# Performance work log

Measured on AMD Instinct MI355X. Metric: run time of the kernel, lower is better.

## Reference

```python
import jax, jax.numpy as jnp
import numpy as np

EPS = 1e-8  # torch F.cosine_similarity norm clamp


def setup_inputs() -> dict:
    key = jax.random.key(0)
    kq, km = jax.random.split(key)
    b, c, h, w = 4, 128, 16, 16
    n_mem = 2000
    query_feature = jax.random.normal(kq, (b, c, h, w), dtype=jnp.float32)
    memory_bank = jax.random.normal(km, (n_mem, b, c, h, w), dtype=jnp.float32)
    return {"query_feature": query_feature, "memory_bank": memory_bank, "k": 20}


def reference(query_feature, memory_bank, k):
    b = query_feature.shape[0]
    n = memory_bank.shape[0]
    # Flatten per-batch features: query [b, D], memory [N, b, D]
    qf = query_feature.reshape(b, -1)
    mf = memory_bank.reshape(n, b, -1)
    # Cosine similarity along feature dim (torch clamps each norm by eps)
    qn = qf / jnp.maximum(jnp.linalg.norm(qf, axis=-1, keepdims=True), EPS)
    mn = mf / jnp.maximum(jnp.linalg.norm(mf, axis=-1, keepdims=True), EPS)
    sims = jnp.einsum('bd,nbd->n', qn, mn) / b  # mean over batch -> [N]
    top_vals, top_idx = jax.lax.top_k(sims, k)
    weights = jax.nn.softmax(top_vals)  # [k]
    # Weighted gather-sum of selected memory items -> [b, c, h, w]
    selected = memory_bank[top_idx]  # [k, b, c, h, w]
    weighted_sum = jnp.einsum('k,kbchw->bchw', weights, selected)
    return weighted_sum
```

## Files before the change

### kernel.cpp

```cpp
#include <hip/hip_runtime.h>
#include <hip/hip_bf16.h>
#include <math.h>

#define BQ    4
#define DIM   32768
#define DIM4  8192
#define ITEM4 32768
#define EPS   1e-8f

__global__ void qnorm_kernel(const float* __restrict__ q, float* __restrict__ qn2) {
    const int b = blockIdx.x;
    const float4* q4 = (const float4*)(q + (size_t)b * DIM);
    float nrm = 0.f;
    for (int i = threadIdx.x; i < DIM4; i += blockDim.x) {
        float4 v = q4[i];
        nrm += v.x * v.x + v.y * v.y + v.z * v.z + v.w * v.w;
    }
    for (int off = 32; off > 0; off >>= 1) nrm += __shfl_down(nrm, off);
    __shared__ float s[16];
    const int wid = threadIdx.x >> 6;
    if ((threadIdx.x & 63) == 0) s[wid] = nrm;
    __syncthreads();
    if (threadIdx.x == 0) {
        float tot = 0.f;
        for (int w = 0; w < (int)(blockDim.x >> 6); ++w) tot += s[w];
        qn2[b] = tot;
    }
}

#define QREG 16
__global__ __launch_bounds__(512) void dot_norm_kernel(
        const float* __restrict__ q, const float* __restrict__ mem,
        float* __restrict__ dotv, float* __restrict__ mn2v, int N) {
    const int b    = blockIdx.x & 3;
    const int bn   = blockIdx.x >> 2;
    const int nblk = gridDim.x >> 2;

    const float4* q4 = (const float4*)(q + (size_t)b * DIM);
    float4 qr[QREG];
    #pragma unroll
    for (int j = 0; j < QREG; ++j) qr[j] = q4[threadIdx.x + j * 512];

    __shared__ float sd[8], sn[8];

    for (int n = bn; n < N; n += nblk) {
        const float4* m4 = (const float4*)(mem + ((size_t)n * BQ + b) * DIM);
        float dot = 0.f, nrm = 0.f;
        #pragma unroll
        for (int j = 0; j < QREG; ++j) {
            float4 m = m4[threadIdx.x + j * 512];
            float4 a = qr[j];
            dot += a.x * m.x + a.y * m.y + a.z * m.z + a.w * m.w;
            nrm += m.x * m.x + m.y * m.y + m.z * m.z + m.w * m.w;
        }
        for (int off = 32; off > 0; off >>= 1) {
            dot += __shfl_down(dot, off);
            nrm += __shfl_down(nrm, off);
        }
        const int wid = threadIdx.x >> 6;
        if ((threadIdx.x & 63) == 0) { sd[wid] = dot; sn[wid] = nrm; }
        __syncthreads();
        if (threadIdx.x == 0) {
            float d = 0.f, n2 = 0.f;
            #pragma unroll
            for (int w = 0; w < 8; ++w) { d += sd[w]; n2 += sn[w]; }
            dotv[n * BQ + b] = d;
            mn2v[n * BQ + b] = n2;
        }
        __syncthreads();
    }
}

__global__ void topk_softmax_kernel(const float* __restrict__ qn2,
                                    const float* __restrict__ dotv,
                                    const float* __restrict__ mn2v,
                                    const int* __restrict__ kp,
                                    float* __restrict__ weights,
                                    int* __restrict__ topidx,
                                    int N) {
    const int k = *kp;
    __shared__ float sims[2048];
    __shared__ float swv[4];
    __shared__ int   swi[4];
    __shared__ float qden[BQ];
    __shared__ float tvals[64];
    __shared__ int   tidxs[64];

    if (threadIdx.x < BQ) qden[threadIdx.x] = fmaxf(sqrtf(qn2[threadIdx.x]), EPS);
    __syncthreads();

    for (int n = threadIdx.x; n < N; n += blockDim.x) {
        float s = 0.f;
        #pragma unroll
        for (int b = 0; b < BQ; ++b) {
            float d  = dotv[n * BQ + b];
            float md = fmaxf(sqrtf(mn2v[n * BQ + b]), EPS);
            s += d / (qden[b] * md);
        }
        sims[n] = s * (1.0f / BQ);
    }
    __syncthreads();

    const int lane = threadIdx.x & 63;
    const int wid  = threadIdx.x >> 6;

    for (int it = 0; it < k; ++it) {
        float best = -INFINITY;
        int bidx = 0x7fffffff;
        for (int n = threadIdx.x; n < N; n += blockDim.x) {
            float v = sims[n];
            if (v > best || (v == best && n < bidx)) { best = v; bidx = n; }
        }
        for (int off = 32; off > 0; off >>= 1) {
            float ov = __shfl_down(best, off);
            int   oi = __shfl_down(bidx, off);
            if (ov > best || (ov == best && oi < bidx)) { best = ov; bidx = oi; }
        }
        if (lane == 0) { swv[wid] = best; swi[wid] = bidx; }
        __syncthreads();
        if (threadIdx.x == 0) {
            float bv = swv[0]; int bi = swi[0];
            #pragma unroll
            for (int w = 1; w < 4; ++w) {
                if (swv[w] > bv || (swv[w] == bv && swi[w] < bi)) { bv = swv[w]; bi = swi[w]; }
            }
            tvals[it] = bv;
            tidxs[it] = bi;
            sims[bi]  = -INFINITY;
        }
        __syncthreads();
    }

    if (threadIdx.x == 0) {
        float m = tvals[0];
        float sum = 0.f;
        for (int i = 0; i < k; ++i) sum += expf(tvals[i] - m);
        float inv = 1.0f / sum;
        for (int i = 0; i < k; ++i) {
            weights[i] = expf(tvals[i] - m) * inv;
            topidx[i]  = tidxs[i];
        }
    }
}

__global__ void wsum_kernel(const float* __restrict__ mem,
                            const float* __restrict__ weights,
                            const int* __restrict__ topidx,
                            const int* __restrict__ kp,
                            float* __restrict__ out) {
    const int k = *kp;
    __shared__ float w[64];
    __shared__ int   id[64];
    if ((int)threadIdx.x < k) {
        w[threadIdx.x]  = weights[threadIdx.x];
        id[threadIdx.x] = topidx[threadIdx.x];
    }
    __syncthreads();
    const int t = blockIdx.x * blockDim.x + threadIdx.x;
    if (t >= ITEM4) return;
    const float4* m4 = (const float4*)mem;
    float4 acc = {0.f, 0.f, 0.f, 0.f};
    for (int j = 0; j < k; ++j) {
        float4 v = m4[(size_t)id[j] * ITEM4 + t];
        float wj = w[j];
        acc.x += wj * v.x; acc.y += wj * v.y; acc.z += wj * v.z; acc.w += wj * v.w;
    }
    ((float4*)out)[t] = acc;
}

extern "C" void kernel_launch(void* const* d_in, const int* in_sizes, int n_in,
                              void* d_out, int out_size, void* d_ws, size_t ws_size,
                              hipStream_t stream) {
    const float* q   = (const float*)d_in[0];
    const float* mem = (const float*)d_in[1];
    const int*   kp  = (const int*)d_in[2];
    float* out = (float*)d_out;

    const int N = in_sizes[1] / (BQ * DIM);

    float* qn2  = (float*)d_ws;
    float* dotv = qn2 + 8;
    float* mn2  = dotv + N * BQ;
    float* wts  = mn2 + N * BQ;
    int*   tidx = (int*)(wts + 64);

    qnorm_kernel<<<BQ, 256, 0, stream>>>(q, qn2);
    dot_norm_kernel<<<2048, 512, 0, stream>>>(q, mem, dotv, mn2, N);
    topk_softmax_kernel<<<1, 256, 0, stream>>>(qn2, dotv, mn2, kp, wts, tidx, N);
    wsum_kernel<<<512, 64, 0, stream>>>(mem, wts, tidx, kp, out);
}
```

Before: 230.5 us.

## Drop per-item block reduction; write per-wave partials and reduce in top-k kernel

The dot/norm kernel no longer reduces across waves through shared memory with two __syncthreads per memory item. Each wave's lane 0 now writes a float2 partial (dot, norm) to workspace, and the top-k kernel sums the 8 partials per (item, batch). The dot kernel grid is halved to 1024 blocks and the top-k kernel is widened to 512 threads. This removes barrier stalls in the bandwidth-bound streaming loop, at the cost of extra partial writes and more work in the single-block top-k kernel.

After: 278.7 us. 20.9% more time.

```diff
diff --git a/kernel.cpp b/kernel.cpp
--- a/kernel.cpp
+++ b/kernel.cpp
@@ -7,6 +7,8 @@
 #define DIM4  8192
 #define ITEM4 32768
 #define EPS   1e-8f
+#define QREG  16
+#define WPB   8
 
 __global__ void qnorm_kernel(const float* __restrict__ q, float* __restrict__ qn2) {
     const int b = blockIdx.x;
@@ -28,20 +30,19 @@
     }
 }
 
-#define QREG 16
 __global__ __launch_bounds__(512) void dot_norm_kernel(
         const float* __restrict__ q, const float* __restrict__ mem,
-        float* __restrict__ dotv, float* __restrict__ mn2v, int N) {
+        float2* __restrict__ part, int N) {
     const int b    = blockIdx.x & 3;
     const int bn   = blockIdx.x >> 2;
     const int nblk = gridDim.x >> 2;
+    const int wid  = threadIdx.x >> 6;
+    const int lane = threadIdx.x & 63;
 
     const float4* q4 = (const float4*)(q + (size_t)b * DIM);
     float4 qr[QREG];
     #pragma unroll
     for (int j = 0; j < QREG; ++j) qr[j] = q4[threadIdx.x + j * 512];
-
-    __shared__ float sd[8], sn[8];
 
     for (int n = bn; n < N; n += nblk) {
         const float4* m4 = (const float4*)(mem + ((size_t)n * BQ + b) * DIM);
@@ -53,35 +54,27 @@
             dot += a.x * m.x + a.y * m.y + a.z * m.z + a.w * m.w;
             nrm += m.x * m.x + m.y * m.y + m.z * m.z + m.w * m.w;
         }
+        #pragma unroll
         for (int off = 32; off > 0; off >>= 1) {
             dot += __shfl_down(dot, off);
             nrm += __shfl_down(nrm, off);
         }
-        const int wid = threadIdx.x >> 6;
-        if ((threadIdx.x & 63) == 0) { sd[wid] = dot; sn[wid] = nrm; }
-        __syncthreads();
-        if (threadIdx.x == 0) {
-            float d = 0.f, n2 = 0.f;
-            #pragma unroll
-            for (int w = 0; w < 8; ++w) { d += sd[w]; n2 += sn[w]; }
-            dotv[n * BQ + b] = d;
-            mn2v[n * BQ + b] = n2;
-        }
-        __syncthreads();
+        if (lane == 0)
+            part[((size_t)n * BQ + b) * WPB + wid] = make_float2(dot, nrm);
     }
 }
 
-__global__ void topk_softmax_kernel(const float* __restrict__ qn2,
-                                    const float* __restrict__ dotv,
-                                    const float* __restrict__ mn2v,
-                                    const int* __restrict__ kp,
-                                    float* __restrict__ weights,
-                                    int* __restrict__ topidx,
-                                    int N) {
+__global__ __launch_bounds__(512) void topk_softmax_kernel(
+        const float* __restrict__ qn2,
+        const float2* __restrict__ part,
+        const int* __restrict__ kp,
+        float* __restrict__ weights,
+        int* __restrict__ topidx,
+        int N) {
     const int k = *kp;
     __shared__ float sims[2048];
-    __shared__ float swv[4];
-    __shared__ int   swi[4];
+    __shared__ float swv[8];
+    __shared__ int   swi[8];
     __shared__ float qden[BQ];
     __shared__ float tvals[64];
     __shared__ int   tidxs[64];
@@ -90,12 +83,18 @@
     __syncthreads();
 
     for (int n = threadIdx.x; n < N; n += blockDim.x) {
+        const float4* p4 = (const float4*)(part + (size_t)n * BQ * WPB);
         float s = 0.f;
         #pragma unroll
         for (int b = 0; b < BQ; ++b) {
-            float d  = dotv[n * BQ + b];
-            float md = fmaxf(sqrtf(mn2v[n * BQ + b]), EPS);
-            s += d / (qden[b] * md);
+            float d = 0.f, m2 = 0.f;
+            #pragma unroll
+            for (int j = 0; j < WPB / 2; ++j) {
+                float4 v = p4[b * (WPB / 2) + j];
+                d  += v.x + v.z;
+                m2 += v.y + v.w;
+            }
+            s += d / (qden[b] * fmaxf(sqrtf(m2), EPS));
         }
         sims[n] = s * (1.0f / BQ);
     }
@@ -111,6 +110,7 @@
             float v = sims[n];
             if (v > best || (v == best && n < bidx)) { best = v; bidx = n; }
         }
+        #pragma unroll
         for (int off = 32; off > 0; off >>= 1) {
             float ov = __shfl_down(best, off);
             int   oi = __shfl_down(bidx, off);
@@ -121,7 +121,7 @@
         if (threadIdx.x == 0) {
             float bv = swv[0]; int bi = swi[0];
             #pragma unroll
-            for (int w = 1; w < 4; ++w) {
+            for (int w = 1; w < 8; ++w) {
                 if (swv[w] > bv || (swv[w] == bv && swi[w] < bi)) { bv = swv[w]; bi = swi[w]; }
             }
             tvals[it] = bv;
@@ -178,14 +178,13 @@
 
     const int N = in_sizes[1] / (BQ * DIM);
 
-    float* qn2  = (float*)d_ws;
-    float* dotv = qn2 + 8;
-    float* mn2  = dotv + N * BQ;
-    float* wts  = mn2 + N * BQ;
-    int*   tidx = (int*)(wts + 64);
+    float*  qn2  = (float*)d_ws;
+    float2* part = (float2*)(qn2 + 8);
+    float*  wts  = (float*)(part + (size_t)N * BQ * WPB);
+    int*    tidx = (int*)(wts + 64);
 
     qnorm_kernel<<<BQ, 256, 0, stream>>>(q, qn2);
-    dot_norm_kernel<<<2048, 512, 0, stream>>>(q, mem, dotv, mn2, N);
-    topk_softmax_kernel<<<1, 256, 0, stream>>>(qn2, dotv, mn2, kp, wts, tidx, N);
+    dot_norm_kernel<<<1024, 512, 0, stream>>>(q, mem, part, N);
+    topk_softmax_kernel<<<1, 512, 0, stream>>>(qn2, part, kp, wts, tidx, N);
     wsum_kernel<<<512, 64, 0, stream>>>(mem, wts, tidx, kp, out);
 }
```
